# Kernel optimization log

Measured on AMD Instinct MI355X. Metric: run time of the kernel, lower is better.

## Reference

```python
import jax, jax.numpy as jnp
import numpy as np

B, S, D = 32, 1024, 512
DMAX = 8

def setup_inputs() -> dict:
    key = jax.random.key(0)
    k1, k2 = jax.random.split(key)
    x = jax.random.normal(k1, (B, S, D), dtype=jnp.float32)
    durations = jax.random.randint(k2, (B, S), 0, DMAX).astype(jnp.float32)
    return {"x": x, "durations": durations, "duration_scale": 1}

def reference(x, durations, duration_scale):
    # round + clamp(min=1), as in the torch module
    d = jnp.clip((durations * duration_scale + 0.5).astype(jnp.int32), 1, None)  # (B,S)
    total_lengths = d.sum(axis=1)                      # (B,)
    max_len = int(jnp.max(total_lengths))              # concrete batch max (matches torch .item())
    ends = jnp.cumsum(d, axis=1)                       # (B,S) exclusive-end offsets
    pos = jnp.arange(max_len, dtype=jnp.int32)         # (T,)
    # src index for each output frame: number of cumulative ends <= pos
    idx = jax.vmap(lambda e: jnp.searchsorted(e, pos, side="right"))(ends)  # (B,T)
    idx = jnp.minimum(idx, S - 1)
    gathered = jnp.take_along_axis(x, idx[:, :, None], axis=1)  # (B,T,D)
    mask = pos[None, :] < total_lengths[:, None]                # (B,T)
    out = jnp.where(mask[:, :, None], gathered, jnp.zeros((), x.dtype))
    return out, total_lengths
```

## Files before the change

### kernel.cpp

```cpp
#include <hip/hip_runtime.h>

#define BATCH 32
#define FPB 16

typedef float f32x4 __attribute__((ext_vector_type(4)));

__global__ void lr_scan_kernel(const float* __restrict__ dur,
                               const unsigned int* __restrict__ scale_raw,
                               float* __restrict__ out_tail,
                               int* __restrict__ totals,
                               int* __restrict__ idxmap,
                               int S, int T) {
    __shared__ int partial[256];
    const int b = blockIdx.x;
    const int tid = threadIdx.x;

    unsigned int u = scale_raw[0];
    float scale = (u < 0x00800000u) ? (float)(int)u : __uint_as_float(u);

    const int PER = S / 256;
    int d[8];
    int lsum = 0;
    const int base = tid * PER;
    for (int k = 0; k < PER; ++k) {
        float f = dur[b * S + base + k];
        int di = (int)(f * scale + 0.5f);
        if (di < 1) di = 1;
        d[k] = di;
        lsum += di;
    }
    partial[tid] = lsum;
    __syncthreads();

    for (int off = 1; off < 256; off <<= 1) {
        int t = (tid >= off) ? partial[tid - off] : 0;
        __syncthreads();
        partial[tid] += t;
        __syncthreads();
    }

    int run = partial[tid] - lsum;
    for (int k = 0; k < PER; ++k) {
        int e = run + d[k];
        for (int j = run; j < e; ++j)
            idxmap[b * T + j] = base + k;
        run = e;
    }

    if (tid == 255) {
        int total = partial[255];
        totals[b] = total;
        out_tail[b] = (float)total;
    }
}

__global__ __launch_bounds__(256) void lr_fill_kernel(
        const f32x4* __restrict__ x4,
        const int* __restrict__ idxmap,
        const int* __restrict__ totals,
        f32x4* __restrict__ out4,
        int S, int T, int d4shift) {
    const int b = blockIdx.y;
    const int lane = threadIdx.x & ((1 << d4shift) - 1);
    const int slot = threadIdx.x >> d4shift;
    const int spb = 256 >> d4shift;
    const int t0 = blockIdx.x * FPB + slot;
    const int total = totals[b];
    const long long xbase = (((long long)b * S) << d4shift) + lane;
    const long long obase = (((long long)b * T) << d4shift) + lane;
    const int* idxrow = idxmap + (long long)b * T;

    #pragma unroll
    for (int k = 0; k < FPB / 2; ++k) {
        int t = t0 + k * spb;
        if (t < T) {
            f32x4 v = {0.f, 0.f, 0.f, 0.f};
            if (t < total) {
                int s = idxrow[t];
                v = x4[xbase + (((long long)s) << d4shift)];
            }
            __builtin_nontemporal_store(v, &out4[obase + (((long long)t) << d4shift)]);
        }
    }
}

extern "C" void kernel_launch(void* const* d_in, const int* in_sizes, int n_in,
                              void* d_out, int out_size, void* d_ws, size_t ws_size,
                              hipStream_t stream) {
    const float* x = (const float*)d_in[0];
    const float* dur = (const float*)d_in[1];
    const unsigned int* scale = (const unsigned int*)d_in[2];

    const int B = BATCH;
    const int D = in_sizes[0] / in_sizes[1];
    const int S = in_sizes[1] / B;
    const int T = (out_size - B) / (B * D);

    float* out = (float*)d_out;
    float* out_tail = out + (long long)B * T * D;

    int* idxmap = (int*)d_ws;
    int* totals = idxmap + (long long)B * T;

    lr_scan_kernel<<<B, 256, 0, stream>>>(dur, scale, out_tail, totals, idxmap, S, T);

    const int D4 = D / 4;
    int d4shift = 0;
    while ((1 << d4shift) < D4) ++d4shift;
    dim3 grid((T + FPB - 1) / FPB, B);
    lr_fill_kernel<<<grid, 256, 0, stream>>>((const f32x4*)x, idxmap, totals,
                                             (f32x4*)out, S, T, d4shift);
}
```

Baseline: 308.8 us.

## Iterate over source rows and scatter repeated frames instead of gathering per frame

Result: slower. 317.3 us (+2.7%).

```diff
diff --git a/kernel.cpp b/kernel.cpp
--- a/kernel.cpp
+++ b/kernel.cpp
@@ -1,7 +1,7 @@
 #include <hip/hip_runtime.h>
 
 #define BATCH 32
-#define FPB 16
+#define ROWS 4
 
 typedef float f32x4 __attribute__((ext_vector_type(4)));
 
@@ -9,8 +9,8 @@
                                const unsigned int* __restrict__ scale_raw,
                                float* __restrict__ out_tail,
                                int* __restrict__ totals,
-                               int* __restrict__ idxmap,
-                               int S, int T) {
+                               int* __restrict__ starts,
+                               int S) {
     __shared__ int partial[256];
     const int b = blockIdx.x;
     const int tid = threadIdx.x;
@@ -41,10 +41,8 @@
 
     int run = partial[tid] - lsum;
     for (int k = 0; k < PER; ++k) {
-        int e = run + d[k];
-        for (int j = run; j < e; ++j)
-            idxmap[b * T + j] = base + k;
-        run = e;
+        starts[b * S + base + k] = run;
+        run += d[k];
     }
 
     if (tid == 255) {
@@ -54,9 +52,9 @@
     }
 }
 
-__global__ __launch_bounds__(256) void lr_fill_kernel(
+__global__ __launch_bounds__(256) void lr_expand_kernel(
         const f32x4* __restrict__ x4,
-        const int* __restrict__ idxmap,
+        const int* __restrict__ starts,
         const int* __restrict__ totals,
         f32x4* __restrict__ out4,
         int S, int T, int d4shift) {
@@ -64,24 +62,40 @@
     const int lane = threadIdx.x & ((1 << d4shift) - 1);
     const int slot = threadIdx.x >> d4shift;
     const int spb = 256 >> d4shift;
-    const int t0 = blockIdx.x * FPB + slot;
+    const int s0 = (blockIdx.x * spb + slot) * ROWS;
     const int total = totals[b];
+    const int* srow = starts + b * S;
     const long long xbase = (((long long)b * S) << d4shift) + lane;
     const long long obase = (((long long)b * T) << d4shift) + lane;
-    const int* idxrow = idxmap + (long long)b * T;
+
+    f32x4 v[ROWS];
+    int st[ROWS + 1];
+    #pragma unroll
+    for (int k = 0; k < ROWS; ++k) {
+        v[k] = x4[xbase + (((long long)(s0 + k)) << d4shift)];
+        st[k] = srow[s0 + k];
+    }
+    st[ROWS] = (s0 + ROWS < S) ? srow[s0 + ROWS] : total;
 
     #pragma unroll
-    for (int k = 0; k < FPB / 2; ++k) {
-        int t = t0 + k * spb;
-        if (t < T) {
-            f32x4 v = {0.f, 0.f, 0.f, 0.f};
-            if (t < total) {
-                int s = idxrow[t];
-                v = x4[xbase + (((long long)s) << d4shift)];
-            }
-            __builtin_nontemporal_store(v, &out4[obase + (((long long)t) << d4shift)]);
-        }
+    for (int k = 0; k < ROWS; ++k) {
+        for (int t = st[k]; t < st[k + 1]; ++t)
+            __builtin_nontemporal_store(v[k], &out4[obase + (((long long)t) << d4shift)]);
     }
+}
+
+__global__ __launch_bounds__(256) void lr_zero_tail_kernel(
+        const int* __restrict__ totals,
+        f32x4* __restrict__ out4,
+        int T, int d4shift) {
+    const int b = blockIdx.y;
+    const int lane = threadIdx.x & ((1 << d4shift) - 1);
+    const int slot = threadIdx.x >> d4shift;
+    const int spb = 256 >> d4shift;
+    const int t = totals[b] + blockIdx.x * spb + slot;
+    if (t >= T) return;
+    f32x4 z = {0.f, 0.f, 0.f, 0.f};
+    __builtin_nontemporal_store(z, &out4[(((long long)(b * T + t)) << d4shift) + lane]);
 }
 
 extern "C" void kernel_launch(void* const* d_in, const int* in_sizes, int n_in,
@@ -99,15 +113,20 @@
     float* out = (float*)d_out;
     float* out_tail = out + (long long)B * T * D;
 
-    int* idxmap = (int*)d_ws;
-    int* totals = idxmap + (long long)B * T;
+    int* starts = (int*)d_ws;
+    int* totals = starts + (long long)B * S;
 
-    lr_scan_kernel<<<B, 256, 0, stream>>>(dur, scale, out_tail, totals, idxmap, S, T);
+    lr_scan_kernel<<<B, 256, 0, stream>>>(dur, scale, out_tail, totals, starts, S);
 
     const int D4 = D / 4;
     int d4shift = 0;
     while ((1 << d4shift) < D4) ++d4shift;
-    dim3 grid((T + FPB - 1) / FPB, B);
-    lr_fill_kernel<<<grid, 256, 0, stream>>>((const f32x4*)x, idxmap, totals,
-                                             (f32x4*)out, S, T, d4shift);
+    const int spb = 256 >> d4shift;
+
+    dim3 egrid(S / (spb * ROWS), B);
+    lr_expand_kernel<<<egrid, 256, 0, stream>>>((const f32x4*)x, starts, totals,
+                                                (f32x4*)out, S, T, d4shift);
+
+    dim3 zgrid((T + spb - 1) / spb, B);
+    lr_zero_tail_kernel<<<zgrid, 256, 0, stream>>>(totals, (f32x4*)out, T, d4shift);
 }
```
